# Performance work log

Measured on AMD Instinct MI355X. Metric: run time of the kernel, lower is better.

## Reference

```python
import jax, jax.numpy as jnp
import numpy as np

EPS = 1e-6

def setup_inputs() -> dict:
    key = jax.random.key(0)
    ks = jax.random.split(key, 6)
    B, C, T, H, W = 4, 512, 32, 32, 32
    x = jax.random.normal(ks[0], (B, C, T, H, W), dtype=jnp.float32)
    gamma = jnp.ones((C,), dtype=jnp.float32)
    beta = jnp.zeros((C,), dtype=jnp.float32)
    s = 1.0 / np.sqrt(C)
    wq = jax.random.normal(ks[1], (C, C), dtype=jnp.float32) * s
    wk = jax.random.normal(ks[2], (C, C), dtype=jnp.float32) * s
    wv = jax.random.normal(ks[3], (C, C), dtype=jnp.float32) * s
    wproj = jax.random.normal(ks[4], (C, C), dtype=jnp.float32) * s
    return {"x": x, "gamma": gamma, "beta": beta, "wq": wq, "wk": wk, "wv": wv, "wproj": wproj}

def reference(x, gamma, beta, wq, wk, wv, wproj):
    B, C, T, H, W = x.shape
    # CausalGroupNorm(num_groups=1): per-(B,T) frame LayerNorm over (C,H,W)
    mean = jnp.mean(x, axis=(1, 3, 4), keepdims=True)
    var = jnp.var(x, axis=(1, 3, 4), keepdims=True)
    h = (x - mean) * jax.lax.rsqrt(var + EPS)
    h = h * gamma[None, :, None, None, None] + beta[None, :, None, None, None]
    # per-pixel temporal sequences: [B*H*W, C, T]
    h = h.transpose(0, 3, 4, 1, 2).reshape(B * H * W, C, T)
    q = jnp.einsum('oc,bct->bot', wq, h)
    k = jnp.einsum('oc,bct->bot', wk, h)
    v = jnp.einsum('oc,bct->bot', wv, h)
    scale = C ** (-0.5)
    attn = jnp.einsum('bct,bcs->bts', q, k) * scale  # [BHW, T, T]
    causal = jnp.tril(jnp.ones((T, T), dtype=bool))
    attn = jnp.where(causal[None], attn, -jnp.inf)
    attn = jax.nn.softmax(attn, axis=-1)
    out = jnp.einsum('bts,bcs->bct', attn, v)
    out = jnp.einsum('oc,bct->bot', wproj, out)
    out = out.reshape(B, H, W, C, T).transpose(0, 3, 4, 1, 2)
    return x + out
```

## Files before the change

kernel.cpp:

```cpp
#include <hip/hip_runtime.h>
#include <hip/hip_bf16.h>

typedef __attribute__((ext_vector_type(4))) float f32x4;
typedef __attribute__((ext_vector_type(8))) short bf16x8;
typedef __attribute__((ext_vector_type(4))) int   i32x4;
typedef __attribute__((ext_vector_type(2))) int   i32x2;

#define HT0 0u
#define GT0 65536u
#define PT0 131072u
#define LG0 135168u
#define K3_LDS 143360
#define QK_SCALE 0.04419417382415922f

static __device__ __forceinline__ unsigned short f2bf(float f) {
    unsigned int u = __builtin_bit_cast(unsigned int, f);
    u += 0x7fffu + ((u >> 16) & 1u);
    return (unsigned short)(u >> 16);
}
static __device__ __forceinline__ float bf2f(unsigned short h) {
    unsigned int u = ((unsigned int)h) << 16;
    return __builtin_bit_cast(float, u);
}
static __device__ __forceinline__ f32x4 fzero() {
    f32x4 v; v[0] = 0.f; v[1] = 0.f; v[2] = 0.f; v[3] = 0.f; return v;
}

__global__ __launch_bounds__(256) void kw_weights(
    const float* __restrict__ wq, const float* __restrict__ wk,
    const float* __restrict__ wproj, const float* __restrict__ wv,
    unsigned short* __restrict__ wqk, unsigned short* __restrict__ wpv)
{
    int bx = blockIdx.x;
    int mat = bx >> 6;
    int tile = bx & 63;
    int i0 = (tile >> 3) * 64, j0 = (tile & 7) * 64;
    const float* A  = mat ? wproj : wq;
    const float* Bm = mat ? wv : wk;
    unsigned short* Out = mat ? wpv : wqk;
    __shared__ float At[16][64];
    __shared__ float Bt[16][64];
    int tid = threadIdx.x;
    int ty = tid >> 4, tx = tid & 15;
    float acc[4][4] = {};
    for (int k0 = 0; k0 < 512; k0 += 16) {
        if (mat == 0) {
#pragma unroll
            for (int r = 0; r < 4; ++r) {
                int idx = r * 256 + tid;
                At[idx >> 6][idx & 63] = A[(size_t)(k0 + (idx >> 6)) * 512 + i0 + (idx & 63)];
            }
        } else {
#pragma unroll
            for (int r = 0; r < 4; ++r) {
                int idx = r * 256 + tid;
                At[idx & 15][idx >> 4] = A[(size_t)(i0 + (idx >> 4)) * 512 + k0 + (idx & 15)];
            }
        }
#pragma unroll
        for (int r = 0; r < 4; ++r) {
            int idx = r * 256 + tid;
            Bt[idx >> 6][idx & 63] = Bm[(size_t)(k0 + (idx >> 6)) * 512 + j0 + (idx & 63)];
        }
        __syncthreads();
#pragma unroll
        for (int kk = 0; kk < 16; ++kk)
#pragma unroll
            for (int i = 0; i < 4; ++i)
#pragma unroll
                for (int j = 0; j < 4; ++j)
                    acc[i][j] += At[kk][ty * 4 + i] * Bt[kk][tx * 4 + j];
        __syncthreads();
    }
#pragma unroll
    for (int i = 0; i < 4; ++i) {
        ushort4 o;
        o.x = f2bf(acc[i][0]); o.y = f2bf(acc[i][1]);
        o.z = f2bf(acc[i][2]); o.w = f2bf(acc[i][3]);
        *(ushort4*)(Out + (size_t)(i0 + ty * 4 + i) * 512 + j0 + tx * 4) = o;
    }
}

__global__ __launch_bounds__(512) void k_transpose_stats(
    const float* __restrict__ x, unsigned short* __restrict__ Hraw, float* __restrict__ sums)
{
    int bx = blockIdx.x;
    int tp = bx & 15;
    int h  = (bx >> 4) & 31;
    int bb = bx >> 9;
    int t0 = tp * 2;
    int tid = threadIdx.x;
    extern __shared__ char lds[];
    float* red = (float*)(lds + 65536);

    int tt = (tid >> 3) & 1;
    int w4 = tid & 7;
    int cb = tid >> 4;
    float s = 0.f, q = 0.f;
    const unsigned int Kt = (unsigned int)tt * 64u + (unsigned int)w4 * 8u;
#pragma unroll
    for (int it = 0; it < 16; ++it) {
        int c = it * 32 + cb;
        float4 v = *(const float4*)(x + (((size_t)(bb * 512 + c)) * 32 + (t0 + tt)) * 1024 + h * 32 + w4 * 4);
        s += v.x + v.y + v.z + v.w;
        q += v.x * v.x + v.y * v.y + v.z * v.z + v.w * v.w;
        unsigned int p0 = ((unsigned int)f2bf(v.y) << 16) | f2bf(v.x);
        unsigned int p1 = ((unsigned int)f2bf(v.w) << 16) | f2bf(v.z);
        unsigned int Kx = ((unsigned int)((c >> 3) & 31)) << 2;
        unsigned int base = (unsigned int)c * 128u + Kt;
        *(unsigned int*)(lds + ((base + 0u) ^ Kx)) = p0;
        *(unsigned int*)(lds + ((base + 4u) ^ Kx)) = p1;
    }
    s += __shfl_xor(s, 1);  q += __shfl_xor(q, 1);
    s += __shfl_xor(s, 2);  q += __shfl_xor(q, 2);
    s += __shfl_xor(s, 4);  q += __shfl_xor(q, 4);
    s += __shfl_xor(s, 16); q += __shfl_xor(q, 16);
    s += __shfl_xor(s, 32); q += __shfl_xor(q, 32);
    int wid = tid >> 6, lane = tid & 63;
    if (lane == 0) { red[wid * 4 + 0] = s; red[wid * 4 + 1] = q; }
    if (lane == 8) { red[wid * 4 + 2] = s; red[wid * 4 + 3] = q; }
    __syncthreads();
    if (tid < 4) {
        float a = 0.f;
#pragma unroll
        for (int w = 0; w < 8; ++w) a += red[w * 4 + tid];
        int f = bb * 32 + t0 + (tid >> 1);
        atomicAdd(&sums[f * 2 + (tid & 1)], a);
    }
#pragma unroll
    for (int rnd = 0; rnd < 8; ++rnd) {
        int row = rnd * 8 + wid;
        int w = row >> 1, ttw = row & 1;
        int c0 = lane * 8;
        unsigned short e[8];
#pragma unroll
        for (int j = 0; j < 8; ++j) {
            int c = c0 + j;
            unsigned int Kx = ((unsigned int)((c >> 3) & 31)) << 2;
            unsigned int off = ((unsigned int)(c * 128 + ttw * 64 + 2 * w)) ^ Kx;
            e[j] = *(const unsigned short*)(lds + off);
        }
        i32x4 ov;
        ov[0] = (int)(((unsigned int)e[1] << 16) | e[0]);
        ov[1] = (int)(((unsigned int)e[3] << 16) | e[2]);
        ov[2] = (int)(((unsigned int)e[5] << 16) | e[4]);
        ov[3] = (int)(((unsigned int)e[7] << 16) | e[6]);
        size_t pix = ((size_t)bb * 32 + h) * 32 + w;
        *(i32x4*)(Hraw + pix * 16384 + (size_t)(t0 + ttw) * 512 + c0) = ov;
    }
}

__global__ void k_finalize(const float* __restrict__ sums, float* __restrict__ mr) {
    int f = threadIdx.x;
    float mean = sums[f * 2] * (1.f / 524288.f);
    float var  = sums[f * 2 + 1] * (1.f / 524288.f) - mean * mean;
    mr[f * 2]     = mean;
    mr[f * 2 + 1] = rsqrtf(var + 1e-6f);
}

static __device__ __forceinline__ void mfma16(f32x4 (&acc)[4][4], const bf16x8 (&a)[4], const bf16x8 (&b)[4]) {
#pragma unroll
    for (int mt = 0; mt < 4; ++mt)
#pragma unroll
        for (int nf = 0; nf < 4; ++nf)
            acc[mt][nf] = __builtin_amdgcn_mfma_f32_16x16x32_bf16(a[mt], b[nf], acc[mt][nf], 0, 0, 0);
}
static __device__ __forceinline__ void load_w4(bf16x8 (&a)[4], const unsigned short* wbase, int k0) {
#pragma unroll
    for (int mt = 0; mt < 4; ++mt)
        a[mt] = *(const bf16x8*)(wbase + (size_t)mt * 16 * 512 + k0);
}
static __device__ __forceinline__ void load_h4(bf16x8 (&b)[4], const char* ldsb, int lo, int hi, int k0) {
#pragma unroll
    for (int nf = 0; nf < 4; ++nf) {
        int row = nf * 16 + lo;
        unsigned off = ((unsigned)(row * 1024 + (k0 + hi * 8) * 2)) ^ (((unsigned)(row & 7)) << 4);
        b[nf] = *(const bf16x8*)(ldsb + off);
    }
}

__global__ __launch_bounds__(512, 2) void k_attn(
    const unsigned short* Hraw,
    const unsigned short* __restrict__ Wqk,
    const unsigned short* __restrict__ Wpv,
    const float* __restrict__ gamma, const float* __restrict__ beta,
    const float* __restrict__ mr,
    unsigned short* OA)
{
    extern __shared__ char lds[];
    int tid = threadIdx.x, wid = tid >> 6, lane = tid & 63;
    int lo = lane & 15, hi = lane >> 4;
    int pix0 = blockIdx.x * 2;
    int b_ = pix0 >> 10;

    {
        const unsigned short* src = Hraw + (size_t)pix0 * 16384;
#pragma unroll
        for (int it = 0; it < 8; ++it) {
            int chunk = it * 512 + tid;
            int row = chunk >> 6;
            int col = chunk & 63;
            int t = row & 31;
            float2 mrv = *(const float2*)(mr + ((b_ << 5) + t) * 2);
            i32x4 v = *(const i32x4*)(src + (size_t)chunk * 8);
            int c0 = col * 8;
            float4 g0 = *(const float4*)(gamma + c0);
            float4 g1 = *(const float4*)(gamma + c0 + 4);
            float4 be0 = *(const float4*)(beta + c0);
            float4 be1 = *(const float4*)(beta + c0 + 4);
            float mu = mrv.x, rs = mrv.y;
            i32x4 ov;
            {
                float xa = bf2f((unsigned short)(v[0] & 0xffff));
                float xb = bf2f((unsigned short)((unsigned int)v[0] >> 16));
                ov[0] = (int)((((unsigned int)f2bf((xb - mu) * (rs * g0.y) + be0.y)) << 16) | f2bf((xa - mu) * (rs * g0.x) + be0.x));
            }
            {
                float xa = bf2f((unsigned short)(v[1] & 0xffff));
                float xb = bf2f((unsigned short)((unsigned int)v[1] >> 16));
                ov[1] = (int)((((unsigned int)f2bf((xb - mu) * (rs * g0.w) + be0.w)) << 16) | f2bf((xa - mu) * (rs * g0.z) + be0.z));
            }
            {
                float xa = bf2f((unsigned short)(v[2] & 0xffff));
                float xb = bf2f((unsigned short)((unsigned int)v[2] >> 16));
                ov[2] = (int)((((unsigned int)f2bf((xb - mu) * (rs * g1.y) + be1.y)) << 16) | f2bf((xa - mu) * (rs * g1.x) + be1.x));
            }
            {
                float xa = bf2f((unsigned short)(v[3] & 0xffff));
                float xb = bf2f((unsigned short)((unsigned int)v[3] >> 16));
                ov[3] = (int)((((unsigned int)f2bf((xb - mu) * (rs * g1.w) + be1.w)) << 16) | f2bf((xa - mu) * (rs * g1.z) + be1.z));
            }
            unsigned off = ((unsigned)(row * 1024 + col * 16)) ^ (((unsigned)(row & 7)) << 4);
            *(i32x4*)(lds + HT0 + off) = ov;
        }
    }
    __syncthreads();

    {
        f32x4 acc[4][4];
#pragma unroll
        for (int mt = 0; mt < 4; ++mt)
#pragma unroll
            for (int nf = 0; nf < 4; ++nf) acc[mt][nf] = fzero();
        const unsigned short* wbase = Wqk + (size_t)(wid * 64 + lo) * 512 + hi * 8;
        bf16x8 a0[4], b0v[4], a1[4], b1v[4];
        load_w4(a0, wbase, 0);
        load_h4(b0v, lds + HT0, lo, hi, 0);
#pragma unroll 2
        for (int kk = 0; kk < 8; ++kk) {
            int k0 = kk * 64;
            load_w4(a1, wbase, k0 + 32);
            load_h4(b1v, lds + HT0, lo, hi, k0 + 32);
            mfma16(acc, a0, b0v);
            if (kk < 7) {
                load_w4(a0, wbase, k0 + 64);
                load_h4(b0v, lds + HT0, lo, hi, k0 + 64);
            }
            mfma16(acc, a1, b1v);
        }
#pragma unroll
        for (int mt = 0; mt < 4; ++mt)
#pragma unroll
            for (int nf = 0; nf < 4; ++nf) {
                int n = nf * 16 + lo;
                int c0 = wid * 64 + mt * 16 + hi * 4;
                unsigned int w0 = ((unsigned int)f2bf(acc[mt][nf][1]) << 16) | f2bf(acc[mt][nf][0]);
                unsigned int w1 = ((unsigned int)f2bf(acc[mt][nf][3]) << 16) | f2bf(acc[mt][nf][2]);
                unsigned off = ((unsigned)(n * 1024 + c0 * 2)) ^ (((unsigned)(n & 7)) << 4);
                i32x2 pv; pv[0] = (int)w0; pv[1] = (int)w1;
                *(i32x2*)(lds + GT0 + off) = pv;
            }
    }
    __syncthreads();

    {
        int p = wid >> 2, tth = (wid >> 1) & 1, sh = wid & 1;
        int arow = p * 32 + tth * 16 + lo;
        int brow = p * 32 + sh * 16 + lo;
        f32x4 acc = fzero();
#pragma unroll 4
        for (int k0 = 0; k0 < 512; k0 += 32) {
            unsigned aoff = ((unsigned)(arow * 1024 + (k0 + hi * 8) * 2)) ^ (((unsigned)(arow & 7)) << 4);
            unsigned boff = ((unsigned)(brow * 1024 + (k0 + hi * 8) * 2)) ^ (((unsigned)(brow & 7)) << 4);
            bf16x8 a = *(const bf16x8*)(lds + HT0 + aoff);
            bf16x8 b = *(const bf16x8*)(lds + GT0 + boff);
            acc = __builtin_amdgcn_mfma_f32_16x16x32_bf16(a, b, acc, 0, 0, 0);
        }
#pragma unroll
        for (int r = 0; r < 4; ++r) {
            int t = tth * 16 + hi * 4 + r;
            int s = sh * 16 + lo;
            *(float*)(lds + LG0 + (unsigned)(((p * 32 + t) * 32 + s) * 4)) = acc[r] * QK_SCALE;
        }
    }
    __syncthreads();

    {
        int row = tid >> 3;
        int p = row >> 5, t = row & 31;
        int s0 = (tid & 7) * 4;
        f32x4 v = *(const f32x4*)(lds + LG0 + (unsigned)(((p * 32 + t) * 32 + s0) * 4));
        float vv0 = (s0 + 0 <= t) ? v[0] : -1e30f;
        float vv1 = (s0 + 1 <= t) ? v[1] : -1e30f;
        float vv2 = (s0 + 2 <= t) ? v[2] : -1e30f;
        float vv3 = (s0 + 3 <= t) ? v[3] : -1e30f;
        float m = fmaxf(fmaxf(vv0, vv1), fmaxf(vv2, vv3));
        m = fmaxf(m, __shfl_xor(m, 1));
        m = fmaxf(m, __shfl_xor(m, 2));
        m = fmaxf(m, __shfl_xor(m, 4));
        float e0 = __expf(vv0 - m), e1 = __expf(vv1 - m), e2 = __expf(vv2 - m), e3 = __expf(vv3 - m);
        float sum = e0 + e1 + e2 + e3;
        sum += __shfl_xor(sum, 1);
        sum += __shfl_xor(sum, 2);
        sum += __shfl_xor(sum, 4);
        float inv = 1.0f / sum;
        unsigned int w0 = ((unsigned int)f2bf(e1 * inv) << 16) | f2bf(e0 * inv);
        unsigned int w1 = ((unsigned int)f2bf(e3 * inv) << 16) | f2bf(e2 * inv);
        unsigned off = ((unsigned)((p * 32 + t) * 64 + s0 * 2)) ^ (((unsigned)(t & 3)) << 4);
        i32x2 pv; pv[0] = (int)w0; pv[1] = (int)w1;
        *(i32x2*)(lds + PT0 + off) = pv;
    }
    __syncthreads();

    {
        f32x4 acc[4][4];
#pragma unroll
        for (int mt = 0; mt < 4; ++mt)
#pragma unroll
            for (int of = 0; of < 4; ++of) acc[mt][of] = fzero();
        const unsigned short* wbase = Wpv + (size_t)(wid * 64 + lo) * 512 + hi * 8;
        bf16x8 a0[4], b0v[4], a1[4], b1v[4];
        load_h4(a0, lds + HT0, lo, hi, 0);
        load_w4(b0v, wbase, 0);
#pragma unroll 2
        for (int kk = 0; kk < 8; ++kk) {
            int k0 = kk * 64;
            load_h4(a1, lds + HT0, lo, hi, k0 + 32);
            load_w4(b1v, wbase, k0 + 32);
            mfma16(acc, a0, b0v);
            if (kk < 7) {
                load_h4(a0, lds + HT0, lo, hi, k0 + 64);
                load_w4(b0v, wbase, k0 + 64);
            }
            mfma16(acc, a1, b1v);
        }
#pragma unroll
        for (int mt = 0; mt < 4; ++mt)
#pragma unroll
            for (int of = 0; of < 4; ++of) {
                int o = wid * 64 + of * 16 + lo;
                int n0 = mt * 16 + hi * 4;
                unsigned int w0 = ((unsigned int)f2bf(acc[mt][of][1]) << 16) | f2bf(acc[mt][of][0]);
                unsigned int w1 = ((unsigned int)f2bf(acc[mt][of][3]) << 16) | f2bf(acc[mt][of][2]);
                unsigned off = ((unsigned)(o * 128 + n0 * 2)) ^ (((unsigned)(o & 7)) << 4);
                i32x2 pv; pv[0] = (int)w0; pv[1] = (int)w1;
                *(i32x2*)(lds + GT0 + off) = pv;
            }
    }
    __syncthreads();

    {
        f32x4 oacc[4][4];
#pragma unroll
        for (int rt = 0; rt < 4; ++rt) {
            int p = rt >> 1;
            int ar = rt * 16 + lo;
            unsigned aoff = ((unsigned)(ar * 64 + hi * 16)) ^ (((unsigned)(ar & 3)) << 4);
            bf16x8 a = *(const bf16x8*)(lds + PT0 + aoff);
#pragma unroll
            for (int of = 0; of < 4; ++of) {
                int o = wid * 64 + of * 16 + lo;
                unsigned boff = ((unsigned)(o * 128 + (p * 32 + hi * 8) * 2)) ^ (((unsigned)(o & 7)) << 4);
                bf16x8 b = *(const bf16x8*)(lds + GT0 + boff);
                oacc[rt][of] = __builtin_amdgcn_mfma_f32_16x16x32_bf16(a, b, fzero(), 0, 0, 0);
            }
        }
        unsigned otb = HT0 + (unsigned)wid * 8192u;
#pragma unroll
        for (int rt = 0; rt < 4; ++rt)
#pragma unroll
            for (int of = 0; of < 4; ++of) {
                int oc = of * 16 + lo;
                int n0 = rt * 16 + hi * 4;
                unsigned int w0 = ((unsigned int)f2bf(oacc[rt][of][1]) << 16) | f2bf(oacc[rt][of][0]);
                unsigned int w1 = ((unsigned int)f2bf(oacc[rt][of][3]) << 16) | f2bf(oacc[rt][of][2]);
                unsigned off = ((unsigned)(oc * 128 + n0 * 2)) ^ (((unsigned)(oc & 7)) << 4);
                i32x2 pv; pv[0] = (int)w0; pv[1] = (int)w1;
                *(i32x2*)(lds + otb + off) = pv;
            }
        int p_ = lane >> 5, ohi = (lane >> 2) & 7, tq = lane & 3;
        size_t pixg = (size_t)(pix0 + p_);
#pragma unroll
        for (int i = 0; i < 8; ++i) {
            int o = i * 8 + ohi;
            unsigned off = ((unsigned)(o * 128 + (p_ * 32 + tq * 8) * 2)) ^ (((unsigned)(o & 7)) << 4);
            i32x4 v = *(const i32x4*)(lds + otb + off);
            *(i32x4*)(OA + pixg * 16384 + (size_t)(wid * 64 + o) * 32 + tq * 8) = v;
        }
    }
}

__global__ __launch_bounds__(512) void k_output(
    const float* __restrict__ x, const unsigned short* __restrict__ OA, float* __restrict__ out)
{
    int bx = blockIdx.x;
    int cbk = bx & 31;
    int h = (bx >> 5) & 31;
    int bb = bx >> 10;
    int c0 = cbk * 16;
    int tid = threadIdx.x;
    extern __shared__ char lds[];

#pragma unroll
    for (int it = 0; it < 4; ++it) {
        int chunk = it * 512 + tid;
        int pix = chunk >> 6;
        int rem = chunk & 63;
        int c = rem >> 2;
        int th = rem & 3;
        size_t pixg = ((size_t)bb * 32 + h) * 32 + pix;
        i32x4 v = *(const i32x4*)(OA + pixg * 16384 + (size_t)(c0 + c) * 32 + th * 8);
        unsigned Kx = ((unsigned)(pix & 31)) << 2;
        unsigned base = (unsigned)(pix * 1024 + c * 64 + th * 16);
        *(unsigned int*)(lds + ((base + 0u) ^ Kx))  = (unsigned int)v[0];
        *(unsigned int*)(lds + ((base + 4u) ^ Kx))  = (unsigned int)v[1];
        *(unsigned int*)(lds + ((base + 8u) ^ Kx))  = (unsigned int)v[2];
        *(unsigned int*)(lds + ((base + 12u) ^ Kx)) = (unsigned int)v[3];
    }
    __syncthreads();
#pragma unroll
    for (int it = 0; it < 8; ++it) {
        int flat4 = it * 512 + tid;
        int c = flat4 >> 8;
        int rem = flat4 & 255;
        int t = rem >> 3, w4 = rem & 7;
        size_t gidx = (((size_t)(bb * 512 + c0 + c)) * 32 + t) * 1024 + h * 32 + w4 * 4;
        float4 xv = *(const float4*)(x + gidx);
        float4 ov;
        {
            int pix = w4 * 4 + 0;
            unsigned off = ((unsigned)(pix * 1024 + c * 64 + t * 2)) ^ (((unsigned)(pix & 31)) << 2);
            ov.x = xv.x + bf2f(*(const unsigned short*)(lds + off));
        }
        {
            int pix = w4 * 4 + 1;
            unsigned off = ((unsigned)(pix * 1024 + c * 64 + t * 2)) ^ (((unsigned)(pix & 31)) << 2);
            ov.y = xv.y + bf2f(*(const unsigned short*)(lds + off));
        }
        {
            int pix = w4 * 4 + 2;
            unsigned off = ((unsigned)(pix * 1024 + c * 64 + t * 2)) ^ (((unsigned)(pix & 31)) << 2);
            ov.z = xv.z + bf2f(*(const unsigned short*)(lds + off));
        }
        {
            int pix = w4 * 4 + 3;
            unsigned off = ((unsigned)(pix * 1024 + c * 64 + t * 2)) ^ (((unsigned)(pix & 31)) << 2);
            ov.w = xv.w + bf2f(*(const unsigned short*)(lds + off));
        }
        *(float4*)(out + gidx) = ov;
    }
}

extern "C" void kernel_launch(void* const* d_in, const int* in_sizes, int n_in,
                              void* d_out, int out_size, void* d_ws, size_t ws_size,
                              hipStream_t stream)
{
    const float* x     = (const float*)d_in[0];
    const float* gamma = (const float*)d_in[1];
    const float* beta  = (const float*)d_in[2];
    const float* wq    = (const float*)d_in[3];
    const float* wk    = (const float*)d_in[4];
    const float* wv    = (const float*)d_in[5];
    const float* wproj = (const float*)d_in[6];
    float* out = (float*)d_out;

    char* ws = (char*)d_ws;
    unsigned short* Hbuf = (unsigned short*)ws;
    unsigned short* Wqk  = (unsigned short*)(ws + 134217728);
    unsigned short* Wpv  = (unsigned short*)(ws + 134217728 + 524288);
    float* sums = (float*)(ws + 134217728 + 1048576);
    float* mr   = (float*)(ws + 134217728 + 1048576 + 1024);

    hipMemsetAsync(sums, 0, 256 * sizeof(float), stream);

    hipFuncSetAttribute((const void*)k_transpose_stats, hipFuncAttributeMaxDynamicSharedMemorySize, 65536 + 128);
    hipFuncSetAttribute((const void*)k_attn, hipFuncAttributeMaxDynamicSharedMemorySize, K3_LDS);

    kw_weights<<<dim3(128), dim3(256), 0, stream>>>(wq, wk, wproj, wv, Wqk, Wpv);
    k_transpose_stats<<<dim3(2048), dim3(512), 65536 + 128, stream>>>(x, Hbuf, sums);
    k_finalize<<<dim3(1), dim3(128), 0, stream>>>(sums, mr);
    k_attn<<<dim3(2048), dim3(512), K3_LDS, stream>>>(Hbuf, Wqk, Wpv, gamma, beta, mr, Hbuf);
    k_output<<<dim3(4096), dim3(512), 32768, stream>>>(x, Hbuf, out);
}
```

Baseline: 572.9 us.

## Fold GroupNorm affine into weights and split attention into a batched GEMM plus light attention kernel

Gamma and the QK scale are folded into the precomputed combined weights, and per-row sums of the weights (times gamma, and against beta) are kept so normalization can be applied after the GEMM using mean and rstd. The per-pixel fused attention kernel is split into a large pipelined GEMM kernel, which uses global_load_lds double buffering and writes G (Wqk·h) and a transposed U (Wpv·h) to global memory, and a small one-wave-per-pixel kernel that does the QK, softmax and PV steps. This is meant to replace the small per-block GEMMs, with their low occupancy and redundant weight reads, by one large efficient GEMM. In exchange it adds extra global traffic for the G and UT intermediates.

```diff
diff --git a/kernel.cpp b/kernel.cpp
--- a/kernel.cpp
+++ b/kernel.cpp
@@ -6,11 +6,6 @@
 typedef __attribute__((ext_vector_type(4))) int   i32x4;
 typedef __attribute__((ext_vector_type(2))) int   i32x2;
 
-#define HT0 0u
-#define GT0 65536u
-#define PT0 131072u
-#define LG0 135168u
-#define K3_LDS 143360
 #define QK_SCALE 0.04419417382415922f
 
 static __device__ __forceinline__ unsigned short f2bf(float f) {
@@ -25,11 +20,15 @@
 static __device__ __forceinline__ f32x4 fzero() {
     f32x4 v; v[0] = 0.f; v[1] = 0.f; v[2] = 0.f; v[3] = 0.f; return v;
 }
+static __device__ __forceinline__ int pack2(float a, float b) {
+    return (int)((((unsigned)f2bf(b)) << 16) | f2bf(a));
+}
 
 __global__ __launch_bounds__(256) void kw_weights(
     const float* __restrict__ wq, const float* __restrict__ wk,
     const float* __restrict__ wproj, const float* __restrict__ wv,
-    unsigned short* __restrict__ wqk, unsigned short* __restrict__ wpv)
+    const float* __restrict__ gamma, const float* __restrict__ beta,
+    unsigned short* __restrict__ Wp, float* __restrict__ rsW, float* __restrict__ bW)
 {
     int bx = blockIdx.x;
     int mat = bx >> 6;
@@ -37,7 +36,6 @@
     int i0 = (tile >> 3) * 64, j0 = (tile & 7) * 64;
     const float* A  = mat ? wproj : wq;
     const float* Bm = mat ? wv : wk;
-    unsigned short* Out = mat ? wpv : wqk;
     __shared__ float At[16][64];
     __shared__ float Bt[16][64];
     int tid = threadIdx.x;
@@ -72,12 +70,29 @@
                     acc[i][j] += At[kk][ty * 4 + i] * Bt[kk][tx * 4 + j];
         __syncthreads();
     }
+    float sc = mat ? 1.0f : QK_SCALE;
 #pragma unroll
     for (int i = 0; i < 4; ++i) {
-        ushort4 o;
-        o.x = f2bf(acc[i][0]); o.y = f2bf(acc[i][1]);
-        o.z = f2bf(acc[i][2]); o.w = f2bf(acc[i][3]);
-        *(ushort4*)(Out + (size_t)(i0 + ty * 4 + i) * 512 + j0 + tx * 4) = o;
+        int o = mat * 512 + i0 + ty * 4 + i;
+        float rsum = 0.f, bsum = 0.f;
+        ushort4 pk;
+        unsigned short e[4];
+#pragma unroll
+        for (int j = 0; j < 4; ++j) {
+            int c = j0 + tx * 4 + j;
+            float w0 = acc[i][j] * sc;
+            float wg = w0 * gamma[c];
+            rsum += wg;
+            bsum += w0 * beta[c];
+            e[j] = f2bf(wg);
+        }
+        pk.x = e[0]; pk.y = e[1]; pk.z = e[2]; pk.w = e[3];
+        *(ushort4*)(Wp + (size_t)o * 512 + j0 + tx * 4) = pk;
+        rsum += __shfl_xor(rsum, 1); bsum += __shfl_xor(bsum, 1);
+        rsum += __shfl_xor(rsum, 2); bsum += __shfl_xor(bsum, 2);
+        rsum += __shfl_xor(rsum, 4); bsum += __shfl_xor(bsum, 4);
+        rsum += __shfl_xor(rsum, 8); bsum += __shfl_xor(bsum, 8);
+        if (tx == 0) { atomicAdd(&rsW[o], rsum); atomicAdd(&bW[o], bsum); }
     }
 }
 
@@ -158,245 +173,229 @@
     mr[f * 2 + 1] = rsqrtf(var + 1e-6f);
 }
 
-static __device__ __forceinline__ void mfma16(f32x4 (&acc)[4][4], const bf16x8 (&a)[4], const bf16x8 (&b)[4]) {
-#pragma unroll
-    for (int mt = 0; mt < 4; ++mt)
-#pragma unroll
-        for (int nf = 0; nf < 4; ++nf)
-            acc[mt][nf] = __builtin_amdgcn_mfma_f32_16x16x32_bf16(a[mt], b[nf], acc[mt][nf], 0, 0, 0);
-}
-static __device__ __forceinline__ void load_w4(bf16x8 (&a)[4], const unsigned short* wbase, int k0) {
-#pragma unroll
-    for (int mt = 0; mt < 4; ++mt)
-        a[mt] = *(const bf16x8*)(wbase + (size_t)mt * 16 * 512 + k0);
-}
-static __device__ __forceinline__ void load_h4(bf16x8 (&b)[4], const char* ldsb, int lo, int hi, int k0) {
-#pragma unroll
-    for (int nf = 0; nf < 4; ++nf) {
-        int row = nf * 16 + lo;
-        unsigned off = ((unsigned)(row * 1024 + (k0 + hi * 8) * 2)) ^ (((unsigned)(row & 7)) << 4);
-        b[nf] = *(const bf16x8*)(ldsb + off);
-    }
-}
-
-__global__ __launch_bounds__(512, 2) void k_attn(
+__global__ __launch_bounds__(512, 4) void k_gemm(
+    const unsigned short* __restrict__ Hraw,
+    const unsigned short* __restrict__ Wp,
+    const float* __restrict__ rsW, const float* __restrict__ bW,
+    const float* __restrict__ mr,
+    unsigned short* __restrict__ G, unsigned short* __restrict__ UT)
+{
+    extern __shared__ char lds[];
+    int d = blockIdx.x;
+    int mtile = (d >> 3) & 7;
+    int strip = (d & 7) | ((d >> 6) << 3);
+    int n0 = strip * 256;
+    int tid = threadIdx.x, wid = tid >> 6, lane = tid & 63;
+    int lo = lane & 15, hi = lane >> 4;
+    int o0w = mtile * 128 + (wid >> 2) * 64;
+    int n0w = (wid & 3) * 64;
+    bool isU = mtile >= 4;
+
+    int srow = tid >> 3;
+    unsigned scol = (((unsigned)(tid & 7)) * 16u) ^ ((((unsigned)srow) & 7u) << 4);
+
+    f32x4 acc[4][4];
+#pragma unroll
+    for (int a = 0; a < 4; ++a)
+#pragma unroll
+        for (int b = 0; b < 4; ++b) acc[a][b] = fzero();
+
+#define STAGE(bufi, kk)                                                                                   \
+    {                                                                                                     \
+        _Pragma("unroll")                                                                                 \
+        for (int r = 0; r < 4; ++r) {                                                                     \
+            const char* src = (const char*)Hraw + (size_t)(n0 + r * 64 + srow) * 1024 + (size_t)(kk) * 128 + scol; \
+            char* dst = lds + (bufi) * 32768 + r * 8192 + wid * 1024;                                     \
+            __builtin_amdgcn_global_load_lds((const __attribute__((address_space(1))) unsigned int*)src,  \
+                                             (__attribute__((address_space(3))) unsigned int*)dst, 16, 0, 0); \
+        }                                                                                                 \
+    }
+
+    STAGE(0, 0);
+    __syncthreads();
+
+    const unsigned short* wbase = Wp + (size_t)(o0w + lo) * 512 + hi * 8;
+    int buf = 0;
+    for (int k = 0; k < 8; ++k) {
+        if (k < 7) STAGE(buf ^ 1, k + 1);
+        const char* B = lds + buf * 32768;
+#pragma unroll
+        for (int half = 0; half < 2; ++half) {
+            bf16x8 wa[4], hb[4];
+#pragma unroll
+            for (int mt = 0; mt < 4; ++mt)
+                wa[mt] = *(const bf16x8*)(wbase + (size_t)mt * 16 * 512 + k * 64 + half * 32);
+#pragma unroll
+            for (int nt = 0; nt < 4; ++nt) {
+                int n = n0w + nt * 16 + lo;
+                unsigned off = (unsigned)(n * 128) + (((unsigned)(half * 64 + hi * 16)) ^ ((((unsigned)n) & 7u) << 4));
+                hb[nt] = *(const bf16x8*)(B + off);
+            }
+            if (!isU) {
+#pragma unroll
+                for (int mt = 0; mt < 4; ++mt)
+#pragma unroll
+                    for (int nt = 0; nt < 4; ++nt)
+                        acc[mt][nt] = __builtin_amdgcn_mfma_f32_16x16x32_bf16(wa[mt], hb[nt], acc[mt][nt], 0, 0, 0);
+            } else {
+#pragma unroll
+                for (int mt = 0; mt < 4; ++mt)
+#pragma unroll
+                    for (int nt = 0; nt < 4; ++nt)
+                        acc[mt][nt] = __builtin_amdgcn_mfma_f32_16x16x32_bf16(hb[nt], wa[mt], acc[mt][nt], 0, 0, 0);
+            }
+        }
+        __syncthreads();
+        buf ^= 1;
+    }
+#undef STAGE
+
+    int n_base = n0 + n0w;
+    if (!isU) {
+#pragma unroll
+        for (int nt = 0; nt < 4; ++nt) {
+            int n = n_base + nt * 16 + lo;
+            int f = ((n >> 15) << 5) | (n & 31);
+            float2 mv = *(const float2*)(mr + f * 2);
+#pragma unroll
+            for (int mt = 0; mt < 4; ++mt) {
+                int ob = o0w + mt * 16 + 4 * hi;
+                f32x4 rw = *(const f32x4*)(rsW + ob);
+                f32x4 bv = *(const f32x4*)(bW + ob);
+                f32x4 a = acc[mt][nt];
+                float v0 = mv.y * (a[0] - mv.x * rw[0]) + bv[0];
+                float v1 = mv.y * (a[1] - mv.x * rw[1]) + bv[1];
+                float v2 = mv.y * (a[2] - mv.x * rw[2]) + bv[2];
+                float v3 = mv.y * (a[3] - mv.x * rw[3]) + bv[3];
+                i32x2 pk; pk[0] = pack2(v0, v1); pk[1] = pack2(v2, v3);
+                *(i32x2*)(G + (size_t)n * 512 + ob) = pk;
+            }
+        }
+    } else {
+#pragma unroll
+        for (int nt = 0; nt < 4; ++nt) {
+            float2 mv[4];
+#pragma unroll
+            for (int i = 0; i < 4; ++i) {
+                int n = n_base + nt * 16 + 4 * hi + i;
+                int f = ((n >> 15) << 5) | (n & 31);
+                mv[i] = *(const float2*)(mr + f * 2);
+            }
+            int ncol = n_base + nt * 16 + 4 * hi;
+#pragma unroll
+            for (int mt = 0; mt < 4; ++mt) {
+                int o = o0w + mt * 16 + lo;
+                float rw = rsW[o], bv = bW[o];
+                f32x4 a = acc[mt][nt];
+                float v0 = mv[0].y * (a[0] - mv[0].x * rw) + bv;
+                float v1 = mv[1].y * (a[1] - mv[1].x * rw) + bv;
+                float v2 = mv[2].y * (a[2] - mv[2].x * rw) + bv;
+                float v3 = mv[3].y * (a[3] - mv[3].x * rw) + bv;
+                i32x2 pk; pk[0] = pack2(v0, v1); pk[1] = pack2(v2, v3);
+                *(i32x2*)(UT + (size_t)(o - 512) * 131072 + ncol) = pk;
+            }
+        }
+    }
+}
+
+__global__ __launch_bounds__(512, 4) void k_attn(
     const unsigned short* Hraw,
-    const unsigned short* __restrict__ Wqk,
-    const unsigned short* __restrict__ Wpv,
+    const unsigned short* __restrict__ G,
+    const unsigned short* __restrict__ UT,
     const float* __restrict__ gamma, const float* __restrict__ beta,
     const float* __restrict__ mr,
     unsigned short* OA)
 {
-    extern __shared__ char lds[];
+    __shared__ char plds[16384];
     int tid = threadIdx.x, wid = tid >> 6, lane = tid & 63;
     int lo = lane & 15, hi = lane >> 4;
-    int pix0 = blockIdx.x * 2;
-    int b_ = pix0 >> 10;
+    int pix = blockIdx.x * 8 + wid;
+    int b_ = pix >> 10;
+    char* pb = plds + wid * 2048;
 
     {
-        const unsigned short* src = Hraw + (size_t)pix0 * 16384;
-#pragma unroll
-        for (int it = 0; it < 8; ++it) {
-            int chunk = it * 512 + tid;
-            int row = chunk >> 6;
-            int col = chunk & 63;
-            int t = row & 31;
-            float2 mrv = *(const float2*)(mr + ((b_ << 5) + t) * 2);
-            i32x4 v = *(const i32x4*)(src + (size_t)chunk * 8);
-            int c0 = col * 8;
-            float4 g0 = *(const float4*)(gamma + c0);
-            float4 g1 = *(const float4*)(gamma + c0 + 4);
-            float4 be0 = *(const float4*)(beta + c0);
-            float4 be1 = *(const float4*)(beta + c0 + 4);
-            float mu = mrv.x, rs = mrv.y;
-            i32x4 ov;
-            {
-                float xa = bf2f((unsigned short)(v[0] & 0xffff));
-                float xb = bf2f((unsigned short)((unsigned int)v[0] >> 16));
-                ov[0] = (int)((((unsigned int)f2bf((xb - mu) * (rs * g0.y) + be0.y)) << 16) | f2bf((xa - mu) * (rs * g0.x) + be0.x));
-            }
-            {
-                float xa = bf2f((unsigned short)(v[1] & 0xffff));
-                float xb = bf2f((unsigned short)((unsigned int)v[1] >> 16));
-                ov[1] = (int)((((unsigned int)f2bf((xb - mu) * (rs * g0.w) + be0.w)) << 16) | f2bf((xa - mu) * (rs * g0.z) + be0.z));
-            }
-            {
-                float xa = bf2f((unsigned short)(v[2] & 0xffff));
-                float xb = bf2f((unsigned short)((unsigned int)v[2] >> 16));
-                ov[2] = (int)((((unsigned int)f2bf((xb - mu) * (rs * g1.y) + be1.y)) << 16) | f2bf((xa - mu) * (rs * g1.x) + be1.x));
-            }
-            {
-                float xa = bf2f((unsigned short)(v[3] & 0xffff));
-                float xb = bf2f((unsigned short)((unsigned int)v[3] >> 16));
-                ov[3] = (int)((((unsigned int)f2bf((xb - mu) * (rs * g1.w) + be1.w)) << 16) | f2bf((xa - mu) * (rs * g1.z) + be1.z));
-            }
-            unsigned off = ((unsigned)(row * 1024 + col * 16)) ^ (((unsigned)(row & 7)) << 4);
-            *(i32x4*)(lds + HT0 + off) = ov;
-        }
-    }
-    __syncthreads();
-
-    {
-        f32x4 acc[4][4];
-#pragma unroll
-        for (int mt = 0; mt < 4; ++mt)
-#pragma unroll
-            for (int nf = 0; nf < 4; ++nf) acc[mt][nf] = fzero();
-        const unsigned short* wbase = Wqk + (size_t)(wid * 64 + lo) * 512 + hi * 8;
-        bf16x8 a0[4], b0v[4], a1[4], b1v[4];
-        load_w4(a0, wbase, 0);
-        load_h4(b0v, lds + HT0, lo, hi, 0);
+        i32x4 z; z[0] = 0; z[1] = 0; z[2] = 0; z[3] = 0;
+        *(i32x4*)(pb + lane * 32) = z;
+        *(i32x4*)(pb + lane * 32 + 16) = z;
+    }
+
+    float2 q0 = *(const float2*)(mr + ((size_t)b_ * 32 + lo) * 2);
+    float2 q1 = *(const float2*)(mr + ((size_t)b_ * 32 + 16 + lo) * 2);
+
+    const unsigned short* Hrow0 = Hraw + ((size_t)pix * 32 + lo) * 512;
+    const unsigned short* Hrow1 = Hrow0 + 16 * 512;
+    const unsigned short* Grow0 = G + ((size_t)pix * 32 + lo) * 512;
+    const unsigned short* Grow1 = Grow0 + 16 * 512;
+
+    f32x4 a00 = fzero(), a10 = fzero(), a11 = fzero();
 #pragma unroll 2
-        for (int kk = 0; kk < 8; ++kk) {
-            int k0 = kk * 64;
-            load_w4(a1, wbase, k0 + 32);
-            load_h4(b1v, lds + HT0, lo, hi, k0 + 32);
-            mfma16(acc, a0, b0v);
-            if (kk < 7) {
-                load_w4(a0, wbase, k0 + 64);
-                load_h4(b0v, lds + HT0, lo, hi, k0 + 64);
-            }
-            mfma16(acc, a1, b1v);
-        }
-#pragma unroll
-        for (int mt = 0; mt < 4; ++mt)
-#pragma unroll
-            for (int nf = 0; nf < 4; ++nf) {
-                int n = nf * 16 + lo;
-                int c0 = wid * 64 + mt * 16 + hi * 4;
-                unsigned int w0 = ((unsigned int)f2bf(acc[mt][nf][1]) << 16) | f2bf(acc[mt][nf][0]);
-                unsigned int w1 = ((unsigned int)f2bf(acc[mt][nf][3]) << 16) | f2bf(acc[mt][nf][2]);
-                unsigned off = ((unsigned)(n * 1024 + c0 * 2)) ^ (((unsigned)(n & 7)) << 4);
-                i32x2 pv; pv[0] = (int)w0; pv[1] = (int)w1;
-                *(i32x2*)(lds + GT0 + off) = pv;
-            }
-    }
-    __syncthreads();
-
-    {
-        int p = wid >> 2, tth = (wid >> 1) & 1, sh = wid & 1;
-        int arow = p * 32 + tth * 16 + lo;
-        int brow = p * 32 + sh * 16 + lo;
-        f32x4 acc = fzero();
+    for (int c0 = 0; c0 < 512; c0 += 32) {
+        int cb = c0 + hi * 8;
+        f32x4 g0 = *(const f32x4*)(gamma + cb);
+        f32x4 g1 = *(const f32x4*)(gamma + cb + 4);
+        f32x4 b0 = *(const f32x4*)(beta + cb);
+        f32x4 b1 = *(const f32x4*)(beta + cb + 4);
+        bf16x8 r0 = *(const bf16x8*)(Hrow0 + cb);
+        bf16x8 r1 = *(const bf16x8*)(Hrow1 + cb);
+        bf16x8 gb0 = *(const bf16x8*)(Grow0 + cb);
+        bf16x8 gb1 = *(const bf16x8*)(Grow1 + cb);
+        bf16x8 h0, h1;
+#pragma unroll
+        for (int j = 0; j < 8; ++j) {
+            float gg = (j < 4) ? g0[j] : g1[j - 4];
+            float bb = (j < 4) ? b0[j] : b1[j - 4];
+            float x0 = bf2f((unsigned short)r0[j]);
+            float x1 = bf2f((unsigned short)r1[j]);
+            h0[j] = (short)f2bf((x0 - q0.x) * (q0.y * gg) + bb);
+            h1[j] = (short)f2bf((x1 - q1.x) * (q1.y * gg) + bb);
+        }
+        a00 = __builtin_amdgcn_mfma_f32_16x16x32_bf16(h0, gb0, a00, 0, 0, 0);
+        a10 = __builtin_amdgcn_mfma_f32_16x16x32_bf16(h1, gb0, a10, 0, 0, 0);
+        a11 = __builtin_amdgcn_mfma_f32_16x16x32_bf16(h1, gb1, a11, 0, 0, 0);
+    }
+
+#pragma unroll
+    for (int i = 0; i < 4; ++i) {
+        bool ok = lo <= 4 * hi + i;
+        float v00 = ok ? a00[i] : -1e30f;
+        float v10 = a10[i];
+        float v11 = ok ? a11[i] : -1e30f;
+
+        float m = v00;
+        m = fmaxf(m, __shfl_xor(m, 1)); m = fmaxf(m, __shfl_xor(m, 2));
+        m = fmaxf(m, __shfl_xor(m, 4)); m = fmaxf(m, __shfl_xor(m, 8));
+        float e = __expf(v00 - m);
+        float s = e;
+        s += __shfl_xor(s, 1); s += __shfl_xor(s, 2); s += __shfl_xor(s, 4); s += __shfl_xor(s, 8);
+        float p00 = e / s;
+
+        float mm = fmaxf(v10, v11);
+        mm = fmaxf(mm, __shfl_xor(mm, 1)); mm = fmaxf(mm, __shfl_xor(mm, 2));
+        mm = fmaxf(mm, __shfl_xor(mm, 4)); mm = fmaxf(mm, __shfl_xor(mm, 8));
+        float e0 = __expf(v10 - mm), e1 = __expf(v11 - mm);
+        float ss = e0 + e1;
+        ss += __shfl_xor(ss, 1); ss += __shfl_xor(ss, 2); ss += __shfl_xor(ss, 4); ss += __shfl_xor(ss, 8);
+        float inv = 1.0f / ss;
+
+        *(unsigned short*)(pb + (4 * hi + i) * 64 + lo * 2) = f2bf(p00);
+        *(unsigned short*)(pb + (16 + 4 * hi + i) * 64 + lo * 2) = f2bf(e0 * inv);
+        *(unsigned short*)(pb + (16 + 4 * hi + i) * 64 + 32 + lo * 2) = f2bf(e1 * inv);
+    }
+
+    bf16x8 pf0 = *(const bf16x8*)(pb + (size_t)lo * 64 + hi * 16);
+    bf16x8 pf1 = *(const bf16x8*)(pb + (size_t)(16 + lo) * 64 + hi * 16);
+
+    unsigned short* oabase = OA + (size_t)pix * 16384;
 #pragma unroll 4
-        for (int k0 = 0; k0 < 512; k0 += 32) {
-            unsigned aoff = ((unsigned)(arow * 1024 + (k0 + hi * 8) * 2)) ^ (((unsigned)(arow & 7)) << 4);
-            unsigned boff = ((unsigned)(brow * 1024 + (k0 + hi * 8) * 2)) ^ (((unsigned)(brow & 7)) << 4);
-            bf16x8 a = *(const bf16x8*)(lds + HT0 + aoff);
-            bf16x8 b = *(const bf16x8*)(lds + GT0 + boff);
-            acc = __builtin_amdgcn_mfma_f32_16x16x32_bf16(a, b, acc, 0, 0, 0);
-        }
-#pragma unroll
-        for (int r = 0; r < 4; ++r) {
-            int t = tth * 16 + hi * 4 + r;
-            int s = sh * 16 + lo;
-            *(float*)(lds + LG0 + (unsigned)(((p * 32 + t) * 32 + s) * 4)) = acc[r] * QK_SCALE;
-        }
-    }
-    __syncthreads();
-
-    {
-        int row = tid >> 3;
-        int p = row >> 5, t = row & 31;
-        int s0 = (tid & 7) * 4;
-        f32x4 v = *(const f32x4*)(lds + LG0 + (unsigned)(((p * 32 + t) * 32 + s0) * 4));
-        float vv0 = (s0 + 0 <= t) ? v[0] : -1e30f;
-        float vv1 = (s0 + 1 <= t) ? v[1] : -1e30f;
-        float vv2 = (s0 + 2 <= t) ? v[2] : -1e30f;
-        float vv3 = (s0 + 3 <= t) ? v[3] : -1e30f;
-        float m = fmaxf(fmaxf(vv0, vv1), fmaxf(vv2, vv3));
-        m = fmaxf(m, __shfl_xor(m, 1));
-        m = fmaxf(m, __shfl_xor(m, 2));
-        m = fmaxf(m, __shfl_xor(m, 4));
-        float e0 = __expf(vv0 - m), e1 = __expf(vv1 - m), e2 = __expf(vv2 - m), e3 = __expf(vv3 - m);
-        float sum = e0 + e1 + e2 + e3;
-        sum += __shfl_xor(sum, 1);
-        sum += __shfl_xor(sum, 2);
-        sum += __shfl_xor(sum, 4);
-        float inv = 1.0f / sum;
-        unsigned int w0 = ((unsigned int)f2bf(e1 * inv) << 16) | f2bf(e0 * inv);
-        unsigned int w1 = ((unsigned int)f2bf(e3 * inv) << 16) | f2bf(e2 * inv);
-        unsigned off = ((unsigned)((p * 32 + t) * 64 + s0 * 2)) ^ (((unsigned)(t & 3)) << 4);
-        i32x2 pv; pv[0] = (int)w0; pv[1] = (int)w1;
-        *(i32x2*)(lds + PT0 + off) = pv;
-    }
-    __syncthreads();
-
-    {
-        f32x4 acc[4][4];
-#pragma unroll
-        for (int mt = 0; mt < 4; ++mt)
-#pragma unroll
-            for (int of = 0; of < 4; ++of) acc[mt][of] = fzero();
-        const unsigned short* wbase = Wpv + (size_t)(wid * 64 + lo) * 512 + hi * 8;
-        bf16x8 a0[4], b0v[4], a1[4], b1v[4];
-        load_h4(a0, lds + HT0, lo, hi, 0);
-        load_w4(b0v, wbase, 0);
-#pragma unroll 2
-        for (int kk = 0; kk < 8; ++kk) {
-            int k0 = kk * 64;
-            load_h4(a1, lds + HT0, lo, hi, k0 + 32);
-            load_w4(b1v, wbase, k0 + 32);
-            mfma16(acc, a0, b0v);
-            if (kk < 7) {
-                load_h4(a0, lds + HT0, lo, hi, k0 + 64);
-                load_w4(b0v, wbase, k0 + 64);
-            }
-            mfma16(acc, a1, b1v);
-        }
-#pragma unroll
-        for (int mt = 0; mt < 4; ++mt)
-#pragma unroll
-            for (int of = 0; of < 4; ++of) {
-                int o = wid * 64 + of * 16 + lo;
-                int n0 = mt * 16 + hi * 4;
-                unsigned int w0 = ((unsigned int)f2bf(acc[mt][of][1]) << 16) | f2bf(acc[mt][of][0]);
-                unsigned int w1 = ((unsigned int)f2bf(acc[mt][of][3]) << 16) | f2bf(acc[mt][of][2]);
-                unsigned off = ((unsigned)(o * 128 + n0 * 2)) ^ (((unsigned)(o & 7)) << 4);
-                i32x2 pv; pv[0] = (int)w0; pv[1] = (int)w1;
-                *(i32x2*)(lds + GT0 + off) = pv;
-            }
-    }
-    __syncthreads();
-
-    {
-        f32x4 oacc[4][4];
-#pragma unroll
-        for (int rt = 0; rt < 4; ++rt) {
-            int p = rt >> 1;
-            int ar = rt * 16 + lo;
-            unsigned aoff = ((unsigned)(ar * 64 + hi * 16)) ^ (((unsigned)(ar & 3)) << 4);
-            bf16x8 a = *(const bf16x8*)(lds + PT0 + aoff);
-#pragma unroll
-            for (int of = 0; of < 4; ++of) {
-                int o = wid * 64 + of * 16 + lo;
-                unsigned boff = ((unsigned)(o * 128 + (p * 32 + hi * 8) * 2)) ^ (((unsigned)(o & 7)) << 4);
-                bf16x8 b = *(const bf16x8*)(lds + GT0 + boff);
-                oacc[rt][of] = __builtin_amdgcn_mfma_f32_16x16x32_bf16(a, b, fzero(), 0, 0, 0);
-            }
-        }
-        unsigned otb = HT0 + (unsigned)wid * 8192u;
-#pragma unroll
-        for (int rt = 0; rt < 4; ++rt)
-#pragma unroll
-            for (int of = 0; of < 4; ++of) {
-                int oc = of * 16 + lo;
-                int n0 = rt * 16 + hi * 4;
-                unsigned int w0 = ((unsigned int)f2bf(oacc[rt][of][1]) << 16) | f2bf(oacc[rt][of][0]);
-                unsigned int w1 = ((unsigned int)f2bf(oacc[rt][of][3]) << 16) | f2bf(oacc[rt][of][2]);
-                unsigned off = ((unsigned)(oc * 128 + n0 * 2)) ^ (((unsigned)(oc & 7)) << 4);
-                i32x2 pv; pv[0] = (int)w0; pv[1] = (int)w1;
-                *(i32x2*)(lds + otb + off) = pv;
-            }
-        int p_ = lane >> 5, ohi = (lane >> 2) & 7, tq = lane & 3;
-        size_t pixg = (size_t)(pix0 + p_);
-#pragma unroll
-        for (int i = 0; i < 8; ++i) {
-            int o = i * 8 + ohi;
-            unsigned off = ((unsigned)(o * 128 + (p_ * 32 + tq * 8) * 2)) ^ (((unsigned)(o & 7)) << 4);
-            i32x4 v = *(const i32x4*)(lds + otb + off);
-            *(i32x4*)(OA + pixg * 16384 + (size_t)(wid * 64 + o) * 32 + tq * 8) = v;
-        }
+    for (int ot = 0; ot < 32; ++ot) {
+        bf16x8 uf = *(const bf16x8*)(UT + (size_t)(ot * 16 + lo) * 131072 + (size_t)pix * 32 + hi * 8);
+        f32x4 o0 = __builtin_amdgcn_mfma_f32_16x16x32_bf16(pf0, uf, fzero(), 0, 0, 0);
+        f32x4 o1 = __builtin_amdgcn_mfma_f32_16x16x32_bf16(pf1, uf, fzero(), 0, 0, 0);
+        int o = ot * 16 + lo;
+        i32x2 pk0; pk0[0] = pack2(o0[0], o0[1]); pk0[1] = pack2(o0[2], o0[3]);
+        i32x2 pk1; pk1[0] = pack2(o1[0], o1[1]); pk1[1] = pack2(o1[2], o1[3]);
+        *(i32x2*)(oabase + (size_t)o * 32 + 4 * hi) = pk0;
+        *(i32x2*)(oabase + (size_t)o * 32 + 16 + 4 * hi) = pk1;
     }
 }
 
@@ -475,20 +474,33 @@
     float* out = (float*)d_out;
 
     char* ws = (char*)d_ws;
+    const size_t OFF_G   = 134217728;
+    const size_t OFF_UT  = 268435456;
+    const size_t OFF_WP  = 402653184;
+    const size_t OFF_RSW = OFF_WP + 1048576;
+    const size_t OFF_BW  = OFF_RSW + 4096;
+    const size_t OFF_SUM = OFF_BW + 4096;
+    const size_t OFF_MR  = OFF_SUM + 1024;
+
     unsigned short* Hbuf = (unsigned short*)ws;
-    unsigned short* Wqk  = (unsigned short*)(ws + 134217728);
-    unsigned short* Wpv  = (unsigned short*)(ws + 134217728 + 524288);
-    float* sums = (float*)(ws + 134217728 + 1048576);
-    float* mr   = (float*)(ws + 134217728 + 1048576 + 1024);
-
-    hipMemsetAsync(sums, 0, 256 * sizeof(float), stream);
+    unsigned short* Gb   = (unsigned short*)(ws + OFF_G);
+    unsigned short* UTb  = (unsigned short*)(ws + OFF_UT);
+    unsigned short* Wp   = (unsigned short*)(ws + OFF_WP);
+    float* rsW  = (float*)(ws + OFF_RSW);
+    float* bW   = (float*)(ws + OFF_BW);
+    float* sums = (float*)(ws + OFF_SUM);
+    float* mr   = (float*)(ws + OFF_MR);
+
+    hipMemsetAsync(rsW, 0, 8192, stream);
+    hipMemsetAsync(sums, 0, 1024, stream);
 
     hipFuncSetAttribute((const void*)k_transpose_stats, hipFuncAttributeMaxDynamicSharedMemorySize, 65536 + 128);
-    hipFuncSetAttribute((const void*)k_attn, hipFuncAttributeMaxDynamicSharedMemorySize, K3_LDS);
-
-    kw_weights<<<dim3(128), dim3(256), 0, stream>>>(wq, wk, wproj, wv, Wqk, Wpv);
+    hipFuncSetAttribute((const void*)k_gemm, hipFuncAttributeMaxDynamicSharedMemorySize, 65536);
+
+    kw_weights<<<dim3(128), dim3(256), 0, stream>>>(wq, wk, wproj, wv, gamma, beta, Wp, rsW, bW);
     k_transpose_stats<<<dim3(2048), dim3(512), 65536 + 128, stream>>>(x, Hbuf, sums);
     k_finalize<<<dim3(1), dim3(128), 0, stream>>>(sums, mr);
-    k_attn<<<dim3(2048), dim3(512), K3_LDS, stream>>>(Hbuf, Wqk, Wpv, gamma, beta, mr, Hbuf);
+    k_gemm<<<dim3(4096), dim3(512), 65536, stream>>>(Hbuf, Wp, rsW, bW, mr, Gb, UTb);
+    k_attn<<<dim3(512), dim3(512), 0, stream>>>(Hbuf, Gb, UTb, gamma, beta, mr, Hbuf);
     k_output<<<dim3(4096), dim3(512), 32768, stream>>>(x, Hbuf, out);
 }
```

Measured after the change: 1.633 ms. 2.85x slower.
